# Kernel tuning notes

Measured on AMD Instinct MI355X. Metric: run time of the kernel, lower is better.

Reference implementation:

```python
import jax, jax.numpy as jnp
import numpy as np

NUM_FEATURES = 256
NUM_PIDS = 5554          # must equal hardcoded FocalLoss ignore_index
NUM_CQ = 50000
N_ROIS = 2048
OIM_SCALAR = 30.0
IGNORE_INDEX = 5554
ALPHA = 1.0
GAMMA = 2.0


def _l2norm(x):
    return x / jnp.linalg.norm(x, axis=-1, keepdims=True)


def setup_inputs() -> dict:
    key = jax.random.key(0)
    k1, k2, k3, k4, k5 = jax.random.split(key, 5)
    inputs = _l2norm(jax.random.normal(k1, (N_ROIS, NUM_FEATURES), jnp.float32))
    # targets >= 1 so label = targets-1 >= 0 (the inds filter is all-True -> static shapes)
    # targets == NUM_PIDS+1 -> label == NUM_PIDS == ignore_index (unlabeled, ignored in loss)
    targets = jax.random.randint(k2, (N_ROIS,), 1, NUM_PIDS + 2, dtype=jnp.int64)
    ious = jax.random.uniform(k3, (N_ROIS,), jnp.float32)
    lut = _l2norm(jax.random.normal(k4, (NUM_PIDS, NUM_FEATURES), jnp.float32))
    cq = _l2norm(jax.random.normal(k5, (NUM_CQ, NUM_FEATURES), jnp.float32))
    return {"inputs": inputs, "lut": lut, "cq": cq, "targets": targets, "ious": ious}


def _focal_loss(logits, labels):
    # F.cross_entropy(reduction='none', ignore_index=IGNORE_INDEX) then
    # focal = alpha * (1-pt)^gamma * ce, mean over ALL samples (ignored -> 0).
    logp = jax.nn.log_softmax(logits, axis=-1)                       # [N, C]
    ce = -jnp.take_along_axis(logp, labels[:, None], axis=1)[:, 0]   # [N]
    ce = jnp.where(labels == IGNORE_INDEX, 0.0, ce)
    pt = jnp.exp(-ce)
    return jnp.mean(ALPHA * (1.0 - pt) ** GAMMA * ce)


def reference(inputs, lut, cq, targets, ious):
    # targets = cat(roi_label); label = targets - 1; inds all True by construction.
    label = targets - 1
    # LOIM forward: logits against labeled LUT and unlabeled circular queue.
    table = jnp.concatenate([lut, cq], axis=0)          # [P+Q, D]
    projected = OIM_SCALAR * (inputs @ table.T)         # [N, P+Q]
    loss_oim = _focal_loss(projected, label)
    return loss_oim, inputs, label
```

## Files before the change

kernel.cpp:

```cpp
#include <hip/hip_runtime.h>
#include <hip/hip_bf16.h>


#define NFEAT 256
#define NROIS 2048
#define NPIDS 5554
#define NCLS 55554
#define NCHUNKS 3473
#define NCH32 1737
#define NCLSP (NCH32 * 32)
#define S2F 43.280851226668906f
#define LN2F 0.6931471805599453f
#define LOFF 524289

typedef float f32x4 __attribute__((ext_vector_type(4)));
typedef short bf16x8 __attribute__((ext_vector_type(8)));
typedef unsigned short u16x8 __attribute__((ext_vector_type(8)));

#if __has_builtin(__builtin_amdgcn_exp2f)
#define EXP2(x) __builtin_amdgcn_exp2f(x)
#else
#define EXP2(x) exp2f(x)
#endif

__device__ __forceinline__ short bfb(float x) {
    return __builtin_bit_cast(short, __float2bfloat16(x));
}

__device__ __forceinline__ void gll16(const void* g, void* l) {
    __builtin_amdgcn_global_load_lds(
        (const __attribute__((address_space(1))) void*)g,
        (__attribute__((address_space(3))) void*)l, 16, 0, 0);
}

__global__ __launch_bounds__(256) void preprocess(
        const float* __restrict__ inputs, const float* __restrict__ lut,
        const float* __restrict__ cq, const int* __restrict__ cand0,
        const int* __restrict__ cand1, unsigned short* __restrict__ tb,
        unsigned short* __restrict__ ab, int* __restrict__ lab,
        float* __restrict__ S, float* __restrict__ f, const int useTB) {
    const int tid = threadIdx.x;
    const int bx = blockIdx.x;

    if (bx == 0) {
        __shared__ int smode;
        __shared__ const int* sT;
        if (tid == 0) {
            const int* T = cand0;
            const unsigned u0 = (unsigned)cand0[0];
            const float f0 = __builtin_bit_cast(float, cand0[0]);
            const bool oki = (u0 >= 1u && u0 <= 6000u);
            const bool okf = (f0 >= 1.0f && f0 <= 6000.0f);
            if (!oki && !okf) T = cand1;
            int mode = 0;
            const unsigned tu0 = (unsigned)T[0];
            const float tf0 = __builtin_bit_cast(float, T[0]);
            if (tu0 >= 1u && tu0 <= 6000u) mode = ((T[1] | T[3] | T[5] | T[7]) == 0) ? 1 : 0;
            else if (tf0 >= 1.0f && tf0 <= 6000.0f) mode = 2;
            smode = mode; sT = T;
        }
        __syncthreads();
        const int mode = smode;
        const int* T = sT;
        for (int j = tid; j < NROIS; j += 256) {
            int tv;
            if (mode == 1)      tv = T[2 * j];
            else if (mode == 2) tv = (int)__builtin_bit_cast(float, T[j]);
            else                tv = T[j];
            const int lv = tv - 1;
            lab[j] = lv;
            f[LOFF + j] = __bfloat162float(__float2bfloat16((float)lv));
        }
        for (int j = tid; j < NROIS + 8; j += 256) S[j] = 0.0f;
    }

    if (bx < 512) {
        const int i = bx * 256 + tid;
        const float4 v = *reinterpret_cast<const float4*>(inputs + (size_t)i * 4);
        float* o = f + 1 + (size_t)i * 4;
        o[0] = v.x; o[1] = v.y; o[2] = v.z; o[3] = v.w;
        if (useTB) {
            ushort4 u;
            u.x = (unsigned short)bfb(v.x); u.y = (unsigned short)bfb(v.y);
            u.z = (unsigned short)bfb(v.z); u.w = (unsigned short)bfb(v.w);
            *reinterpret_cast<ushort4*>(ab + (size_t)i * 4) = u;
        }
    }

    if (useTB) {
        const size_t LUTN = (size_t)NPIDS * NFEAT;
        const size_t TOT  = (size_t)NCLS * NFEAT;
        const size_t TOTP = (size_t)NCLSP * NFEAT;
        const size_t stride = (size_t)gridDim.x * 256 * 8;
        for (size_t e = ((size_t)bx * 256 + tid) * 8; e < TOTP; e += stride) {
            u16x8 o = {0, 0, 0, 0, 0, 0, 0, 0};
            if (e < TOT) {
                const float* sp = (e < LUTN) ? (lut + e) : (cq + (e - LUTN));
                const float4 a = *reinterpret_cast<const float4*>(sp);
                const float4 b = *reinterpret_cast<const float4*>(sp + 4);
                o[0] = (unsigned short)bfb(a.x); o[1] = (unsigned short)bfb(a.y);
                o[2] = (unsigned short)bfb(a.z); o[3] = (unsigned short)bfb(a.w);
                o[4] = (unsigned short)bfb(b.x); o[5] = (unsigned short)bfb(b.y);
                o[6] = (unsigned short)bfb(b.z); o[7] = (unsigned short)bfb(b.w);
            }
            *reinterpret_cast<u16x8*>(tb + e) = o;
        }
    }
}

template <bool TB>
__global__ __launch_bounds__(256, 2) void main_gemm4(const float* __restrict__ inputs,
                                                     const unsigned short* __restrict__ tb,
                                                     const unsigned short* __restrict__ ab,
                                                     const float* __restrict__ lut,
                                                     const float* __restrict__ cq,
                                                     float* __restrict__ S) {
    __shared__ short ldsb[3][8192];
    const int tid = threadIdx.x;
    const int lane = tid & 63;
    const int wave = tid >> 6;
    const int cs = blockIdx.x & 63;
    const int rg = blockIdx.x >> 6;
    const int rowbase = rg * 256 + wave * 64;
    const int li = lane & 15;
    const int q = lane >> 4;
    const int xorli = 4 * (li & 7);

    bf16x8 afrag[4][8];
    if constexpr (TB) {
        #pragma unroll
        for (int s = 0; s < 4; s++) {
            const unsigned short* rp = ab + (size_t)(rowbase + s * 16 + li) * NFEAT + q * 8;
            #pragma unroll
            for (int kc = 0; kc < 8; kc++)
                afrag[s][kc] = *reinterpret_cast<const bf16x8*>(rp + kc * 32);
        }
    } else {
        #pragma unroll
        for (int s = 0; s < 4; s++) {
            const float* rp = inputs + (size_t)(rowbase + s * 16 + li) * NFEAT + q * 8;
            #pragma unroll
            for (int kc = 0; kc < 8; kc++) {
                const float4 x0 = *reinterpret_cast<const float4*>(rp + kc * 32);
                const float4 x1 = *reinterpret_cast<const float4*>(rp + kc * 32 + 4);
                bf16x8 a;
                a[0] = bfb(x0.x); a[1] = bfb(x0.y); a[2] = bfb(x0.z); a[3] = bfb(x0.w);
                a[4] = bfb(x1.x); a[5] = bfb(x1.y); a[6] = bfb(x1.z); a[7] = bfb(x1.w);
                afrag[s][kc] = a;
            }
        }
    }

    float sums[4][4] = {{0.f,0.f,0.f,0.f},{0.f,0.f,0.f,0.f},
                        {0.f,0.f,0.f,0.f},{0.f,0.f,0.f,0.f}};
    char* const lbase = (char*)&ldsb[0][0];

    if constexpr (TB) {
        const int cc0 = tid >> 5;
        const int uo = ((tid & 31) ^ (4 * (cc0 & 7))) * 8;
        const int ldd = wave * 1024;
        const int cA = (cs * NCH32) >> 6;
        const int cB = ((cs + 1) * NCH32) >> 6;
        const int NB = cB - cA;
        const unsigned short* psrc = tb + (size_t)(cA * 32 + cc0) * NFEAT + uo;
        int ob0 = 0, ob1 = 16384, ob2 = 32768;

        #pragma unroll
        for (int k = 0; k < 4; k++)
            gll16(psrc + (size_t)(8 * k) * NFEAT, lbase + ob0 + ldd + k * 4096);
        psrc += (size_t)32 * NFEAT;
        if (NB > 1) {
            #pragma unroll
            for (int k = 0; k < 4; k++)
                gll16(psrc + (size_t)(8 * k) * NFEAT, lbase + ob1 + ldd + k * 4096);
            psrc += (size_t)32 * NFEAT;
        }

        for (int i = 0; i < NB; ++i) {
            if (i + 1 < NB) asm volatile("s_waitcnt vmcnt(4)\n\ts_barrier" ::: "memory");
            else            asm volatile("s_waitcnt vmcnt(0)\n\ts_barrier" ::: "memory");
            if (i + 2 < NB) {
                #pragma unroll
                for (int k = 0; k < 4; k++)
                    gll16(psrc + (size_t)(8 * k) * NFEAT, lbase + ob2 + ldd + k * 4096);
                psrc += (size_t)32 * NFEAT;
            }
            #pragma unroll
            for (int h = 0; h < 2; h++) {
                const int cc = h * 16 + li;
                bf16x8 bfr[8];
                #pragma unroll
                for (int kc = 0; kc < 8; kc++) {
                    const int slot = cc * 32 + ((q + 4 * kc) ^ xorli);
                    bfr[kc] = *reinterpret_cast<const bf16x8*>(lbase + ob0 + slot * 16);
                }
                f32x4 acc[4] = {{0.f,0.f,0.f,0.f},{0.f,0.f,0.f,0.f},
                                {0.f,0.f,0.f,0.f},{0.f,0.f,0.f,0.f}};
                __builtin_amdgcn_s_setprio(1);
                #pragma unroll
                for (int kc = 0; kc < 8; kc++) {
                    acc[0] = __builtin_amdgcn_mfma_f32_16x16x32_bf16(afrag[0][kc], bfr[kc], acc[0], 0, 0, 0);
                    acc[1] = __builtin_amdgcn_mfma_f32_16x16x32_bf16(afrag[1][kc], bfr[kc], acc[1], 0, 0, 0);
                    acc[2] = __builtin_amdgcn_mfma_f32_16x16x32_bf16(afrag[2][kc], bfr[kc], acc[2], 0, 0, 0);
                    acc[3] = __builtin_amdgcn_mfma_f32_16x16x32_bf16(afrag[3][kc], bfr[kc], acc[3], 0, 0, 0);
                }
                __builtin_amdgcn_s_setprio(0);
                #pragma unroll
                for (int s = 0; s < 4; s++)
                    #pragma unroll
                    for (int r = 0; r < 4; r++)
                        sums[s][r] += EXP2(S2F * acc[s][r] - S2F);
            }
            const int t = ob0; ob0 = ob1; ob1 = ob2; ob2 = t;
        }
    } else {
        short* fb = (short*)lbase;
        const int s0 = tid, s1 = tid + 256;
        const int cc0 = s0 >> 5, cc1 = s1 >> 5;
        const int uo0 = ((s0 & 31) ^ (4 * (cc0 & 7))) * 8;
        const int uo1 = ((s1 & 31) ^ (4 * (cc1 & 7))) * 8;
        const int cA = (cs * NCHUNKS) >> 6;
        const int cB = ((cs + 1) * NCHUNKS) >> 6;
        {
            int n0 = cA * 16 + cc0; n0 = n0 < (NCLS - 1) ? n0 : (NCLS - 1);
            int n1 = cA * 16 + cc1; n1 = n1 < (NCLS - 1) ? n1 : (NCLS - 1);
            const float* r0 = ((n0 < NPIDS) ? lut + (size_t)n0 * NFEAT
                                            : cq + (size_t)(n0 - NPIDS) * NFEAT) + uo0;
            const float* r1 = ((n1 < NPIDS) ? lut + (size_t)n1 * NFEAT
                                            : cq + (size_t)(n1 - NPIDS) * NFEAT) + uo1;
            const float4 a0 = *reinterpret_cast<const float4*>(r0);
            const float4 a1 = *reinterpret_cast<const float4*>(r0 + 4);
            const float4 b0 = *reinterpret_cast<const float4*>(r1);
            const float4 b1 = *reinterpret_cast<const float4*>(r1 + 4);
            bf16x8 v0, v1;
            v0[0]=bfb(a0.x); v0[1]=bfb(a0.y); v0[2]=bfb(a0.z); v0[3]=bfb(a0.w);
            v0[4]=bfb(a1.x); v0[5]=bfb(a1.y); v0[6]=bfb(a1.z); v0[7]=bfb(a1.w);
            v1[0]=bfb(b0.x); v1[1]=bfb(b0.y); v1[2]=bfb(b0.z); v1[3]=bfb(b0.w);
            v1[4]=bfb(b1.x); v1[5]=bfb(b1.y); v1[6]=bfb(b1.z); v1[7]=bfb(b1.w);
            *reinterpret_cast<bf16x8*>(&fb[s0 * 8]) = v0;
            *reinterpret_cast<bf16x8*>(&fb[s1 * 8]) = v1;
        }
        __syncthreads();
        int cur = 0;
        for (int ci = cA; ci < cB; ++ci) {
            const bool pf = (ci + 1 < cB);
            float4 f0a, f0b, f1a, f1b;
            if (pf) {
                int n0 = (ci + 1) * 16 + cc0; n0 = n0 < (NCLS - 1) ? n0 : (NCLS - 1);
                int n1 = (ci + 1) * 16 + cc1; n1 = n1 < (NCLS - 1) ? n1 : (NCLS - 1);
                const float* r0 = ((n0 < NPIDS) ? lut + (size_t)n0 * NFEAT
                                                : cq + (size_t)(n0 - NPIDS) * NFEAT) + uo0;
                const float* r1 = ((n1 < NPIDS) ? lut + (size_t)n1 * NFEAT
                                                : cq + (size_t)(n1 - NPIDS) * NFEAT) + uo1;
                f0a = *reinterpret_cast<const float4*>(r0);
                f0b = *reinterpret_cast<const float4*>(r0 + 4);
                f1a = *reinterpret_cast<const float4*>(r1);
                f1b = *reinterpret_cast<const float4*>(r1 + 4);
            }
            f32x4 acc[4] = {{0.f,0.f,0.f,0.f},{0.f,0.f,0.f,0.f},
                            {0.f,0.f,0.f,0.f},{0.f,0.f,0.f,0.f}};
            #pragma unroll
            for (int kc = 0; kc < 8; kc++) {
                const int slot = li * 32 + ((q + 4 * kc) ^ xorli);
                const bf16x8 b = *reinterpret_cast<const bf16x8*>(&fb[cur * 4096 + slot * 8]);
                acc[0] = __builtin_amdgcn_mfma_f32_16x16x32_bf16(afrag[0][kc], b, acc[0], 0, 0, 0);
                acc[1] = __builtin_amdgcn_mfma_f32_16x16x32_bf16(afrag[1][kc], b, acc[1], 0, 0, 0);
                acc[2] = __builtin_amdgcn_mfma_f32_16x16x32_bf16(afrag[2][kc], b, acc[2], 0, 0, 0);
                acc[3] = __builtin_amdgcn_mfma_f32_16x16x32_bf16(afrag[3][kc], b, acc[3], 0, 0, 0);
            }
            const float valid = ((ci * 16 + li) < NCLS) ? 1.0f : 0.0f;
            #pragma unroll
            for (int s = 0; s < 4; s++)
                #pragma unroll
                for (int r = 0; r < 4; r++)
                    sums[s][r] += valid * EXP2(S2F * (acc[s][r] - 1.0f));
            if (pf) {
                bf16x8 p0, p1;
                p0[0]=bfb(f0a.x); p0[1]=bfb(f0a.y); p0[2]=bfb(f0a.z); p0[3]=bfb(f0a.w);
                p0[4]=bfb(f0b.x); p0[5]=bfb(f0b.y); p0[6]=bfb(f0b.z); p0[7]=bfb(f0b.w);
                p1[0]=bfb(f1a.x); p1[1]=bfb(f1a.y); p1[2]=bfb(f1a.z); p1[3]=bfb(f1a.w);
                p1[4]=bfb(f1b.x); p1[5]=bfb(f1b.y); p1[6]=bfb(f1b.z); p1[7]=bfb(f1b.w);
                *reinterpret_cast<bf16x8*>(&fb[(cur ^ 1) * 4096 + s0 * 8]) = p0;
                *reinterpret_cast<bf16x8*>(&fb[(cur ^ 1) * 4096 + s1 * 8]) = p1;
            }
            __syncthreads();
            cur ^= 1;
        }
    }

    #pragma unroll
    for (int s = 0; s < 4; s++)
        #pragma unroll
        for (int r = 0; r < 4; r++) {
            float v = sums[s][r];
            v += __shfl_xor(v, 1); v += __shfl_xor(v, 2);
            v += __shfl_xor(v, 4); v += __shfl_xor(v, 8);
            sums[s][r] = v;
        }
    if (li == 0) {
        #pragma unroll
        for (int s = 0; s < 4; s++)
            #pragma unroll
            for (int r = 0; r < 4; r++)
                atomicAdd(&S[rowbase + s * 16 + q * 4 + r], sums[s][r]);
    }
}

__global__ __launch_bounds__(256) void focal_final(const float* __restrict__ inputs,
                                                   const float* __restrict__ lut,
                                                   const int* __restrict__ lab,
                                                   const float* __restrict__ S,
                                                   float* __restrict__ loss_acc,
                                                   unsigned int* __restrict__ cnt,
                                                   float* __restrict__ f) {
    const int wave = threadIdx.x >> 6;
    const int lane = threadIdx.x & 63;
    const int row = blockIdx.x * 4 + wave;
    const int label = lab[row];
    const bool valid = (label >= 0 && label < NPIDS);
    const int lr = valid ? label : 0;
    const float4 a = *reinterpret_cast<const float4*>(inputs + (size_t)row * NFEAT + lane * 4);
    const float4 b = *reinterpret_cast<const float4*>(lut + (size_t)lr * NFEAT + lane * 4);
    float v = a.x * b.x + a.y * b.y + a.z * b.z + a.w * b.w;
    #pragma unroll
    for (int m = 1; m < 64; m <<= 1) v += __shfl_xor(v, m);

    __shared__ float red[4];
    if (lane == 0) {
        float fo = 0.0f;
        if (valid) {
            const float l2 = v * S2F;
            const float lse2 = S2F + log2f(S[row]);
            float ce = fmaxf((lse2 - l2) * LN2F, 0.0f);
            const float pt = EXP2(l2 - lse2);
            const float om = 1.0f - pt;
            fo = om * om * ce;
        }
        red[wave] = fo;
    }
    __syncthreads();
    if (threadIdx.x == 0) {
        atomicAdd(loss_acc, red[0] + red[1] + red[2] + red[3]);
        __threadfence();
        const unsigned done = atomicAdd(cnt, 1u) + 1u;
        if (done == gridDim.x) {
            const float tot = atomicAdd(loss_acc, 0.0f);
            f[0] = tot * (1.0f / NROIS);
        }
    }
}

extern "C" void kernel_launch(void* const* d_in, const int* in_sizes, int n_in,
                              void* d_out, int out_size, void* d_ws, size_t ws_size,
                              hipStream_t stream) {
    const float* inputs = (const float*)d_in[0];
    const float* lut    = (const float*)d_in[1];
    const float* cq     = (const float*)d_in[2];
    const int*   cand0  = (const int*)d_in[3];
    const int*   cand1  = (const int*)((n_in > 4) ? d_in[4] : d_in[3]);
    float* f = (float*)d_out;

    const size_t TBB = (size_t)NCLSP * NFEAT * 2;
    const size_t ABB = (size_t)NROIS * NFEAT * 2;
    char* ws = (char*)d_ws;
    const bool useTB = ws_size >= TBB + ABB + 32768;

    unsigned short* tb = useTB ? (unsigned short*)ws : nullptr;
    unsigned short* ab = useTB ? (unsigned short*)(ws + TBB) : nullptr;
    float* S = useTB ? (float*)(ws + TBB + ABB) : (float*)ws;
    float* loss_acc    = S + NROIS;
    unsigned int* cnt  = (unsigned int*)(S + NROIS + 1);
    int* lab           = (int*)(S + NROIS + 8);

    preprocess<<<useTB ? 4096 : 512, 256, 0, stream>>>(inputs, lut, cq, cand0, cand1,
                                                       tb, ab, lab, S, f, useTB ? 1 : 0);
    if (useTB) main_gemm4<true><<<512, 256, 0, stream>>>(inputs, tb, ab, lut, cq, S);
    else       main_gemm4<false><<<512, 256, 0, stream>>>(inputs, tb, ab, lut, cq, S);
    focal_final<<<512, 256, 0, stream>>>(inputs, lut, lab, S, loss_acc, cnt, f);
}
```

Measured before the change: 171.5 us.

## Give each wave private double-buffered LDS staging to remove block barriers

```diff
diff --git a/kernel.cpp b/kernel.cpp
--- a/kernel.cpp
+++ b/kernel.cpp
@@ -7,8 +7,7 @@
 #define NPIDS 5554
 #define NCLS 55554
 #define NCHUNKS 3473
-#define NCH32 1737
-#define NCLSP (NCH32 * 32)
+#define NCLSP 55584
 #define S2F 43.280851226668906f
 #define LN2F 0.6931471805599453f
 #define LOFF 524289
@@ -109,13 +108,13 @@
 }
 
 template <bool TB>
-__global__ __launch_bounds__(256, 2) void main_gemm4(const float* __restrict__ inputs,
+__global__ __launch_bounds__(256, 2) void main_gemm8(const float* __restrict__ inputs,
                                                      const unsigned short* __restrict__ tb,
                                                      const unsigned short* __restrict__ ab,
                                                      const float* __restrict__ lut,
                                                      const float* __restrict__ cq,
                                                      float* __restrict__ S) {
-    __shared__ short ldsb[3][8192];
+    __shared__ char lds[65536];
     const int tid = threadIdx.x;
     const int lane = tid & 63;
     const int wave = tid >> 6;
@@ -125,9 +124,13 @@
     const int li = lane & 15;
     const int q = lane >> 4;
     const int xorli = 4 * (li & 7);
-
-    bf16x8 afrag[4][8];
+    char* const lbase = &lds[0];
+
+    float sums[4][4] = {{0.f,0.f,0.f,0.f},{0.f,0.f,0.f,0.f},
+                        {0.f,0.f,0.f,0.f},{0.f,0.f,0.f,0.f}};
+
     if constexpr (TB) {
+        bf16x8 afrag[4][8];
         #pragma unroll
         for (int s = 0; s < 4; s++) {
             const unsigned short* rp = ab + (size_t)(rowbase + s * 16 + li) * NFEAT + q * 8;
@@ -135,7 +138,63 @@
             for (int kc = 0; kc < 8; kc++)
                 afrag[s][kc] = *reinterpret_cast<const bf16x8*>(rp + kc * 32);
         }
+        asm volatile("s_waitcnt vmcnt(0)" ::: "memory");
+
+        const int hi = lane >> 5;
+        const int lo = lane & 31;
+        const int u0 = lo ^ (4 * hi);
+        char* const wb = lbase + wave * 16384;
+
+        const int cA = (cs * NCHUNKS) >> 6;
+        const int cB = ((cs + 1) * NCHUNKS) >> 6;
+        const int NB = cB - cA;
+
+        #define STAGE(c16, buf)                                                     \
+            {                                                                        \
+                _Pragma("unroll")                                                    \
+                for (int g = 0; g < 8; g++) {                                        \
+                    const unsigned short* src = tb +                                 \
+                        (size_t)((c16) * 16 + 2 * g + hi) * NFEAT +                  \
+                        (u0 ^ (8 * (g & 3))) * 8;                                    \
+                    gll16(src, wb + (buf) * 8192 + g * 1024);                        \
+                }                                                                    \
+            }
+
+        STAGE(cA, 0);
+        for (int i = 0; i < NB; ++i) {
+            if (i + 1 < NB) {
+                STAGE(cA + i + 1, (i + 1) & 1);
+                asm volatile("s_waitcnt vmcnt(8)" ::: "memory");
+            } else {
+                asm volatile("s_waitcnt vmcnt(0)" ::: "memory");
+            }
+            char* const cbuf = wb + (i & 1) * 8192;
+            bf16x8 bfr[8];
+            #pragma unroll
+            for (int kc = 0; kc < 8; kc++) {
+                const int slot = li * 32 + ((q + 4 * kc) ^ xorli);
+                bfr[kc] = *reinterpret_cast<const bf16x8*>(cbuf + slot * 16);
+            }
+            f32x4 acc[4] = {{0.f,0.f,0.f,0.f},{0.f,0.f,0.f,0.f},
+                            {0.f,0.f,0.f,0.f},{0.f,0.f,0.f,0.f}};
+            __builtin_amdgcn_s_setprio(1);
+            #pragma unroll
+            for (int kc = 0; kc < 8; kc++) {
+                acc[0] = __builtin_amdgcn_mfma_f32_16x16x32_bf16(afrag[0][kc], bfr[kc], acc[0], 0, 0, 0);
+                acc[1] = __builtin_amdgcn_mfma_f32_16x16x32_bf16(afrag[1][kc], bfr[kc], acc[1], 0, 0, 0);
+                acc[2] = __builtin_amdgcn_mfma_f32_16x16x32_bf16(afrag[2][kc], bfr[kc], acc[2], 0, 0, 0);
+                acc[3] = __builtin_amdgcn_mfma_f32_16x16x32_bf16(afrag[3][kc], bfr[kc], acc[3], 0, 0, 0);
+            }
+            __builtin_amdgcn_s_setprio(0);
+            #pragma unroll
+            for (int s = 0; s < 4; s++)
+                #pragma unroll
+                for (int r = 0; r < 4; r++)
+                    sums[s][r] += EXP2(S2F * acc[s][r] - S2F);
+        }
+        #undef STAGE
     } else {
+        bf16x8 afrag[4][8];
         #pragma unroll
         for (int s = 0; s < 4; s++) {
             const float* rp = inputs + (size_t)(rowbase + s * 16 + li) * NFEAT + q * 8;
@@ -149,71 +208,6 @@
                 afrag[s][kc] = a;
             }
         }
-    }
-
-    float sums[4][4] = {{0.f,0.f,0.f,0.f},{0.f,0.f,0.f,0.f},
-                        {0.f,0.f,0.f,0.f},{0.f,0.f,0.f,0.f}};
-    char* const lbase = (char*)&ldsb[0][0];
-
-    if constexpr (TB) {
-        const int cc0 = tid >> 5;
-        const int uo = ((tid & 31) ^ (4 * (cc0 & 7))) * 8;
-        const int ldd = wave * 1024;
-        const int cA = (cs * NCH32) >> 6;
-        const int cB = ((cs + 1) * NCH32) >> 6;
-        const int NB = cB - cA;
-        const unsigned short* psrc = tb + (size_t)(cA * 32 + cc0) * NFEAT + uo;
-        int ob0 = 0, ob1 = 16384, ob2 = 32768;
-
-        #pragma unroll
-        for (int k = 0; k < 4; k++)
-            gll16(psrc + (size_t)(8 * k) * NFEAT, lbase + ob0 + ldd + k * 4096);
-        psrc += (size_t)32 * NFEAT;
-        if (NB > 1) {
-            #pragma unroll
-            for (int k = 0; k < 4; k++)
-                gll16(psrc + (size_t)(8 * k) * NFEAT, lbase + ob1 + ldd + k * 4096);
-            psrc += (size_t)32 * NFEAT;
-        }
-
-        for (int i = 0; i < NB; ++i) {
-            if (i + 1 < NB) asm volatile("s_waitcnt vmcnt(4)\n\ts_barrier" ::: "memory");
-            else            asm volatile("s_waitcnt vmcnt(0)\n\ts_barrier" ::: "memory");
-            if (i + 2 < NB) {
-                #pragma unroll
-                for (int k = 0; k < 4; k++)
-                    gll16(psrc + (size_t)(8 * k) * NFEAT, lbase + ob2 + ldd + k * 4096);
-                psrc += (size_t)32 * NFEAT;
-            }
-            #pragma unroll
-            for (int h = 0; h < 2; h++) {
-                const int cc = h * 16 + li;
-                bf16x8 bfr[8];
-                #pragma unroll
-                for (int kc = 0; kc < 8; kc++) {
-                    const int slot = cc * 32 + ((q + 4 * kc) ^ xorli);
-                    bfr[kc] = *reinterpret_cast<const bf16x8*>(lbase + ob0 + slot * 16);
-                }
-                f32x4 acc[4] = {{0.f,0.f,0.f,0.f},{0.f,0.f,0.f,0.f},
-                                {0.f,0.f,0.f,0.f},{0.f,0.f,0.f,0.f}};
-                __builtin_amdgcn_s_setprio(1);
-                #pragma unroll
-                for (int kc = 0; kc < 8; kc++) {
-                    acc[0] = __builtin_amdgcn_mfma_f32_16x16x32_bf16(afrag[0][kc], bfr[kc], acc[0], 0, 0, 0);
-                    acc[1] = __builtin_amdgcn_mfma_f32_16x16x32_bf16(afrag[1][kc], bfr[kc], acc[1], 0, 0, 0);
-                    acc[2] = __builtin_amdgcn_mfma_f32_16x16x32_bf16(afrag[2][kc], bfr[kc], acc[2], 0, 0, 0);
-                    acc[3] = __builtin_amdgcn_mfma_f32_16x16x32_bf16(afrag[3][kc], bfr[kc], acc[3], 0, 0, 0);
-                }
-                __builtin_amdgcn_s_setprio(0);
-                #pragma unroll
-                for (int s = 0; s < 4; s++)
-                    #pragma unroll
-                    for (int r = 0; r < 4; r++)
-                        sums[s][r] += EXP2(S2F * acc[s][r] - S2F);
-            }
-            const int t = ob0; ob0 = ob1; ob1 = ob2; ob2 = t;
-        }
-    } else {
         short* fb = (short*)lbase;
         const int s0 = tid, s1 = tid + 256;
         const int cc0 = s0 >> 5, cc1 = s1 >> 5;
@@ -374,7 +368,7 @@
 
     preprocess<<<useTB ? 4096 : 512, 256, 0, stream>>>(inputs, lut, cq, cand0, cand1,
                                                        tb, ab, lab, S, f, useTB ? 1 : 0);
-    if (useTB) main_gemm4<true><<<512, 256, 0, stream>>>(inputs, tb, ab, lut, cq, S);
-    else       main_gemm4<false><<<512, 256, 0, stream>>>(inputs, tb, ab, lut, cq, S);
+    if (useTB) main_gemm8<true><<<512, 256, 0, stream>>>(inputs, tb, ab, lut, cq, S);
+    else       main_gemm8<false><<<512, 256, 0, stream>>>(inputs, tb, ab, lut, cq, S);
     focal_final<<<512, 256, 0, stream>>>(inputs, lut, lab, S, loss_acc, cnt, f);
 }
```

Result: slower. 176.4 us (+2.8%).
